# Kernel optimization log

Measured on AMD Instinct MI355X. Metric: run time of the kernel, lower is better.

The kernel has to match this reference:

```python
import jax, jax.numpy as jnp
import numpy as np

# static config (matches init_kwargs)
B = 16
S = 32          # patch grid side
td = 2          # tile_dim
ts = td * td    # tile size
T = (S // td) ** 2
R = 1           # register tokens
U = 1           # tile_comp_size
P = S * S
N = R + P
KC = T * U
K = R + KC
D = 768
H = 12
DH = D // H
HID = 32        # CPB hidden


def setup_inputs() -> dict:
    key = jax.random.key(0)
    ks = jax.random.split(key, 11)
    sc = 0.02
    x = jax.random.normal(ks[0], (B, N, D), jnp.float32)
    logit_w = jax.random.normal(ks[1], (U, D), jnp.float32) * sc
    q_w = jax.random.normal(ks[2], (D, D), jnp.float32) * sc
    kv_w = jax.random.normal(ks[3], (2 * D, D), jnp.float32) * sc
    out_w = jax.random.normal(ks[4], (D, D), jnp.float32) * sc
    out_b = jax.random.normal(ks[5], (D,), jnp.float32) * sc
    cpb_w1 = jax.random.normal(ks[6], (HID, 3), jnp.float32) * 0.5
    cpb_b1 = jax.random.normal(ks[7], (HID,), jnp.float32) * sc
    cpb_w2 = jax.random.normal(ks[8], (H, HID), jnp.float32) * 0.1
    cpb_b2 = jax.random.normal(ks[9], (H,), jnp.float32) * sc
    u_pos = jax.random.normal(ks[10], (1, U, 3), jnp.float32) * sc
    # query patch positions [qx, qy, 0] on the SxS grid (row-major)
    coords = np.arange(S, dtype=np.float32)
    gy, gx = np.meshgrid(coords, coords, indexing='ij')
    P_pos = np.stack([gx.ravel(), gy.ravel(), np.zeros(P, np.float32)], axis=-1)[:, None, :]
    # per-tile centers [cx, cy, 0], tile index t = row_tile*(S//td)+col_tile
    tc = np.arange(S // td, dtype=np.float32) * td + (td - 1) / 2.0
    ty, tx = np.meshgrid(tc, tc, indexing='ij')
    tile_centers = np.stack([tx.ravel(), ty.ravel(), np.zeros(T, np.float32)], axis=-1)[:, None, :]
    return {
        'x': x, 'logit_w': logit_w, 'q_w': q_w, 'kv_w': kv_w,
        'out_w': out_w, 'out_b': out_b,
        'cpb_w1': cpb_w1, 'cpb_b1': cpb_b1, 'cpb_w2': cpb_w2, 'cpb_b2': cpb_b2,
        'u_pos': u_pos,
        'P_pos': jnp.asarray(P_pos), 'tile_centers': jnp.asarray(tile_centers),
    }


def _cpb_bias(P_pos, tile_centers, u_pos, cpb_w1, cpb_b1, cpb_w2, cpb_b2, dtype):
    # anchors: tile center + tied per-U offset -> [KC, 3]
    k_pos = (tile_centers + u_pos).reshape(KC, 3)
    delta = P_pos - k_pos[None, :, :].reshape(1, KC, 3)  # [P, KC, 3]
    dxy, s_feat = delta[..., :2], delta[..., 2:]
    phi_xy = jnp.sign(dxy) * jnp.log1p(jnp.abs(dxy))
    feats = jnp.concatenate([phi_xy, -s_feat], axis=-1)  # [P, KC, 3]
    h = jax.nn.gelu(feats @ cpb_w1.T + cpb_b1, approximate=False)
    out_ctx = h @ cpb_w2.T + cpb_b2  # [P, KC, H]
    bias = jnp.zeros((N, K, H), dtype).at[R:, R:, :].set(out_ctx.astype(dtype))
    return bias.transpose(2, 0, 1)  # [H, N, K]


def reference(x, logit_w, q_w, kv_w, out_w, out_b,
              cpb_w1, cpb_b1, cpb_w2, cpb_b2, u_pos, P_pos, tile_centers):
    Bx = x.shape[0]
    # --- tiled softmax-weighted compression ---
    patch = x[:, R:, :].reshape(Bx, S // td, td, S // td, td, D)
    tiled = patch.transpose(0, 1, 3, 2, 4, 5).reshape(Bx, T, ts, D)  # [B,T,ts,D]
    scores = jnp.einsum('btsd,ud->btsu', tiled, logit_w)             # [B,T,ts,U]
    w = jax.nn.softmax(scores.astype(jnp.float32).transpose(0, 1, 3, 2), axis=-1)
    w = w.astype(scores.dtype)                                       # [B,T,U,ts]
    ctx_learn = jnp.einsum('btus,btsd->btud', w, tiled).reshape(Bx, T * U, D)
    ctx = jnp.concatenate([x[:, :R, :], ctx_learn], axis=1)          # [B,K,D]
    # --- projections ---
    q = jnp.einsum('bnd,ed->bne', x, q_w).reshape(Bx, N, H, DH).transpose(0, 2, 1, 3)
    kv = jnp.einsum('bkd,ed->bke', ctx, kv_w).reshape(Bx, K, 2, H, DH)
    k = kv[:, :, 0].transpose(0, 2, 1, 3)  # [B,H,K,DH]
    v = kv[:, :, 1].transpose(0, 2, 1, 3)
    # --- CPB additive bias + SDPA ---
    bias = _cpb_bias(P_pos, tile_centers, u_pos, cpb_w1, cpb_b1, cpb_w2, cpb_b2, x.dtype)
    scale = DH ** -0.5
    logits = jnp.einsum('bhnd,bhkd->bhnk', q, k) * scale + bias[None]
    attn = jax.nn.softmax(logits, axis=-1)
    o = jnp.einsum('bhnk,bhkd->bhnd', attn, v).transpose(0, 2, 1, 3).reshape(Bx, N, D)
    return o @ out_w.T + out_b
```

## Files before the change

### kernel.cpp

```cpp
#include <hip/hip_runtime.h>
#include <math.h>

namespace {
constexpr int BB   = 16;
constexpr int SS   = 32;
constexpr int TT   = 256;
constexpr int PP   = 1024;
constexpr int NTOK = 1025;
constexpr int KCC  = 256;
constexpr int KTOK = 257;
constexpr int DD   = 768;
constexpr int HH   = 12;
constexpr int DHH  = 64;
constexpr int BNP  = 1040;
}

typedef _Float16 f16x8 __attribute__((ext_vector_type(8)));
typedef _Float16 f16x2 __attribute__((ext_vector_type(2)));
typedef float f32x4 __attribute__((ext_vector_type(4)));

#define GLOAD_LDS16(gsrc, ldst)                                               \
  __builtin_amdgcn_global_load_lds(                                           \
      (const __attribute__((address_space(1))) unsigned int*)(gsrc),          \
      (__attribute__((address_space(3))) unsigned int*)(ldst), 16, 0, 0)

__global__ __launch_bounds__(256) void cvt_weights_kernel(
    const float* __restrict__ q_w, const float* __restrict__ kv_w,
    const float* __restrict__ out_w,
    _Float16* __restrict__ qwh, _Float16* __restrict__ kvwh,
    _Float16* __restrict__ owh) {
  constexpr int NQ = DD * DD;
  constexpr int NK = 2 * DD * DD;
  const int i = (blockIdx.x * 256 + threadIdx.x) * 8;
  const float* src;
  _Float16* dst;
  int off;
  float scale = 1.0f;
  if (i < NQ) { src = q_w; dst = qwh; off = i; scale = 0.125f; }
  else if (i < NQ + NK) { src = kv_w; dst = kvwh; off = i - NQ; }
  else if (i < NQ + NK + NQ) { src = out_w; dst = owh; off = i - NQ - NK; }
  else return;
  const float4 a = *(const float4*)(src + off);
  const float4 b = *(const float4*)(src + off + 4);
  f16x8 o;
  o[0] = (_Float16)(a.x * scale); o[1] = (_Float16)(a.y * scale);
  o[2] = (_Float16)(a.z * scale); o[3] = (_Float16)(a.w * scale);
  o[4] = (_Float16)(b.x * scale); o[5] = (_Float16)(b.y * scale);
  o[6] = (_Float16)(b.z * scale); o[7] = (_Float16)(b.w * scale);
  *(f16x8*)(dst + off) = o;
}

__global__ __launch_bounds__(256) void ctx_kernel(
    const float* __restrict__ x, const float* __restrict__ logit_w,
    _Float16* __restrict__ ctxh, _Float16* __restrict__ xh) {
  const int blk = blockIdx.x;
  const int b = blk >> 8;
  const int t = blk & 255;
  const int tid = threadIdx.x;
  const int lane = tid & 63;
  const int w = tid >> 6;
  const float* xb = x + (size_t)b * NTOK * DD;
  _Float16* xhb = xh + (size_t)b * NTOK * DD;

  int prow[4];
#pragma unroll
  for (int s = 0; s < 4; ++s)
    prow[s] = 1 + ((t >> 4) * 2 + (s >> 1)) * SS + ((t & 15) * 2 + (s & 1));

  float sv[3][4];
  float part[4] = {0.f, 0.f, 0.f, 0.f};
#pragma unroll
  for (int it = 0; it < 3; ++it) {
    const int d = tid + 256 * it;
    const float lw = logit_w[d];
#pragma unroll
    for (int s = 0; s < 4; ++s) {
      const float xv = xb[(size_t)prow[s] * DD + d];
      sv[it][s] = xv;
      part[s] += xv * lw;
      xhb[(size_t)prow[s] * DD + d] = (_Float16)xv;
    }
  }

#pragma unroll
  for (int dd = 1; dd < 64; dd <<= 1)
#pragma unroll
    for (int s = 0; s < 4; ++s) part[s] += __shfl_xor(part[s], dd, 64);
  __shared__ float wred[4][4];
  if (lane == 0)
#pragma unroll
    for (int s = 0; s < 4; ++s) wred[w][s] = part[s];
  __syncthreads();
  float score[4];
#pragma unroll
  for (int s = 0; s < 4; ++s)
    score[s] = wred[0][s] + wred[1][s] + wred[2][s] + wred[3][s];

  const float mx = fmaxf(fmaxf(score[0], score[1]), fmaxf(score[2], score[3]));
  float e[4], sum = 0.f;
#pragma unroll
  for (int s = 0; s < 4; ++s) { e[s] = expf(score[s] - mx); sum += e[s]; }
  const float inv = 1.f / sum;
#pragma unroll
  for (int s = 0; s < 4; ++s) e[s] *= inv;

  _Float16* crow = ctxh + ((size_t)b * KTOK + 1 + t) * DD;
#pragma unroll
  for (int it = 0; it < 3; ++it) {
    const int d = tid + 256 * it;
    float acc = 0.f;
#pragma unroll
    for (int s = 0; s < 4; ++s) acc += e[s] * sv[it][s];
    crow[d] = (_Float16)acc;
  }
  if (t == 0) {
    _Float16* dst = ctxh + (size_t)b * KTOK * DD;
#pragma unroll
    for (int it = 0; it < 3; ++it) {
      const int d = tid + 256 * it;
      const float xv = xb[d];
      dst[d] = (_Float16)xv;
      xhb[d] = (_Float16)xv;
    }
  }
}

template <int OUTF16>
__global__ __launch_bounds__(256) void gemm_f16_kernel(
    const _Float16* __restrict__ A, const _Float16* __restrict__ W,
    const float* __restrict__ bias, void* __restrict__ Cout,
    int M, int Nout, int gx) {
  constexpr int BK = 64;
  __shared__ _Float16 As[128 * BK];
  __shared__ _Float16 Ws[128 * BK];

  const int tid = threadIdx.x;
  const int lane = tid & 63;
  const int w = tid >> 6;
  const int fr = lane & 15;
  const int g = lane >> 4;
  const int awm = (w >> 1) * 64;
  const int awn = (w & 1) * 64;

  const int nwg = gridDim.x;
  const int q8 = nwg >> 3, r8 = nwg & 7;
  const int xcd = blockIdx.x & 7;
  const int base = (xcd < r8) ? xcd * (q8 + 1) : r8 * (q8 + 1) + (xcd - r8) * q8;
  const int wg = base + (blockIdx.x >> 3);
  const int row0 = (wg / gx) * 128;
  const int col0 = (wg % gx) * 128;

  const int srow = lane >> 3;
  const int schunk = (lane & 7) ^ (srow & 7);

  f32x4 acc[4][4];
#pragma unroll
  for (int i = 0; i < 4; ++i)
#pragma unroll
    for (int j = 0; j < 4; ++j) acc[i][j] = (f32x4){0.f, 0.f, 0.f, 0.f};

  for (int k0 = 0; k0 < 768; k0 += BK) {
    __syncthreads();
#pragma unroll
    for (int c = 0; c < 4; ++c) {
      const int rl = w * 32 + c * 8 + srow;
      int ga = row0 + rl;
      ga = ga < M ? ga : M - 1;
      GLOAD_LDS16(A + (size_t)ga * 768 + k0 + schunk * 8, &As[(w * 32 + c * 8) * BK]);
      GLOAD_LDS16(W + (size_t)(col0 + rl) * 768 + k0 + schunk * 8,
                  &Ws[(w * 32 + c * 8) * BK]);
    }
    __syncthreads();

#pragma unroll
    for (int ks = 0; ks < 2; ++ks) {
      f16x8 af[4], bf[4];
#pragma unroll
      for (int i = 0; i < 4; ++i) {
        const int row = awm + i * 16 + fr;
        af[i] = *(const f16x8*)&As[row * BK + (((ks * 4 + g) ^ (fr & 7)) * 8)];
      }
#pragma unroll
      for (int j = 0; j < 4; ++j) {
        const int row = awn + j * 16 + fr;
        bf[j] = *(const f16x8*)&Ws[row * BK + (((ks * 4 + g) ^ (fr & 7)) * 8)];
      }
#pragma unroll
      for (int i = 0; i < 4; ++i)
#pragma unroll
        for (int j = 0; j < 4; ++j)
          acc[i][j] = __builtin_amdgcn_mfma_f32_16x16x32_f16(af[i], bf[j], acc[i][j], 0, 0, 0);
    }
  }

#pragma unroll
  for (int i = 0; i < 4; ++i) {
    const int rbase = row0 + awm + i * 16 + g * 4;
#pragma unroll
    for (int reg = 0; reg < 4; ++reg) {
      const int gr = rbase + reg;
      if (gr >= M) continue;
      if constexpr (OUTF16) {
        _Float16* crow = (_Float16*)Cout + (size_t)gr * Nout + col0;
#pragma unroll
        for (int j = 0; j < 4; ++j)
          crow[awn + j * 16 + fr] = (_Float16)acc[i][j][reg];
      } else {
        float* crow = (float*)Cout + (size_t)gr * Nout + col0;
#pragma unroll
        for (int j = 0; j < 4; ++j) {
          const int gc = awn + j * 16 + fr;
          crow[gc] = acc[i][j][reg] + bias[col0 + gc];
        }
      }
    }
  }
}

__global__ __launch_bounds__(256) void cpb_kernel(
    const float* __restrict__ P_pos, const float* __restrict__ tile_centers,
    const float* __restrict__ u_pos,
    const float* __restrict__ w1, const float* __restrict__ b1,
    const float* __restrict__ w2, const float* __restrict__ b2,
    float* __restrict__ biasK) {
  const int idx = blockIdx.x * 256 + threadIdx.x;
  const int c = idx >> 10;
  const int p = idx & 1023;

  const float px = P_pos[p * 3 + 0], py = P_pos[p * 3 + 1], pz = P_pos[p * 3 + 2];
  const float kx = tile_centers[c * 3 + 0] + u_pos[0];
  const float ky = tile_centers[c * 3 + 1] + u_pos[1];
  const float kz = tile_centers[c * 3 + 2] + u_pos[2];
  const float dx = px - kx, dy = py - ky, dz = pz - kz;
  const float fx = copysignf(log1pf(fabsf(dx)), dx);
  const float fy = copysignf(log1pf(fabsf(dy)), dy);
  const float fz = -dz;

  float outh[HH];
#pragma unroll
  for (int h = 0; h < HH; ++h) outh[h] = b2[h];
  for (int j = 0; j < 32; ++j) {
    float hj = fx * w1[j * 3 + 0] + fy * w1[j * 3 + 1] + fz * w1[j * 3 + 2] + b1[j];
    hj = 0.5f * hj * (1.f + erff(hj * 0.70710678118654752f));
#pragma unroll
    for (int h = 0; h < HH; ++h) outh[h] += hj * w2[h * 32 + j];
  }
#pragma unroll
  for (int h = 0; h < HH; ++h) {
    float* row = biasK + ((size_t)h * KCC + c) * BNP;
    row[1 + p] = outh[h];
    if (p == 0) row[0] = 0.f;
    if (p < BNP - 1 - PP) row[1 + PP + p] = 0.f;
  }
}

__global__ __launch_bounds__(512) void attn_mfma_kernel(
    const _Float16* __restrict__ qf, const _Float16* __restrict__ kvf,
    const float* __restrict__ biasK, _Float16* __restrict__ of) {
  __shared__ _Float16 Kh[4][64 * 64];
  __shared__ _Float16 Vt[4][64 * 64];
  __shared__ _Float16 Pl[8][16 * 64];

  const int tid = threadIdx.x;
  const int lane = tid & 63;
  const int w = tid >> 6;
  const int fr = lane & 15;
  const int g = lane >> 4;

  const int xcd = blockIdx.x & 7;
  const int s = blockIdx.x >> 3;
  const int grp = xcd + 8 * (s >> 1);
  const int half = s & 1;
  const int b = grp / HH;
  const int h = grp % HH;

  if (tid < 256) {
    const int ksr = tid >> 2;
    const int kc0 = (tid & 3) * 2;
    const int s7 = ksr & 7;
#pragma unroll
    for (int kt = 0; kt < 4; ++kt) {
      const int key = kt * 64 + ksr;
      const _Float16* srcK = kvf + ((size_t)b * KTOK + key) * (2 * DD) + h * DHH;
      *(f16x8*)&Kh[kt][ksr * 64 + ((kc0 ^ s7) * 8)] = *(const f16x8*)(srcK + kc0 * 8);
      *(f16x8*)&Kh[kt][ksr * 64 + (((kc0 + 1) ^ s7) * 8)] = *(const f16x8*)(srcK + kc0 * 8 + 8);
    }
  } else {
    const int t2 = tid - 256;
    const int vkp = t2 & 31;
    const int vdh = (t2 >> 5) * 8;
#pragma unroll
    for (int kt = 0; kt < 4; ++kt) {
      const int kv0 = kt * 64 + 2 * vkp;
      const f16x8 va = *(const f16x8*)(kvf + ((size_t)b * KTOK + kv0) * (2 * DD) + DD + h * DHH + vdh);
      const f16x8 vbv = *(const f16x8*)(kvf + ((size_t)b * KTOK + kv0 + 1) * (2 * DD) + DD + h * DHH + vdh);
#pragma unroll
      for (int e = 0; e < 8; ++e) {
        const int d = vdh + e;
        f16x2 pr; pr[0] = va[e]; pr[1] = vbv[e];
        *(f16x2*)&Vt[kt][d * 64 + (((vkp >> 2) ^ (d & 7)) * 8) + 2 * (vkp & 3)] = pr;
      }
    }
  }

  const _Float16* k256p = kvf + ((size_t)b * KTOK + 256) * (2 * DD) + h * DHH;
  f16x8 kt256[2];
#pragma unroll
  for (int ks = 0; ks < 2; ++ks)
    kt256[ks] = *(const f16x8*)(k256p + ks * 32 + g * 8);
  float v256[4];
#pragma unroll
  for (int j = 0; j < 4; ++j) v256[j] = (float)k256p[DD + j * 16 + fr];

  __syncthreads();

  const int cstart = half ? 33 : 0;
  const int cend = half ? 65 : 33;
  for (int c = cstart + w; c < cend; c += 8) {
    const int qc = c * 16;

    const int qrow = min(qc + fr, NTOK - 1);
    const _Float16* qsrc = qf + ((size_t)b * NTOK + qrow) * DD + h * DHH;
    f16x8 qa[2];
#pragma unroll
    for (int ks = 0; ks < 2; ++ks)
      qa[ks] = *(const f16x8*)(qsrc + ks * 32 + g * 8);

    float mr_[4], lr_[4];
#pragma unroll
    for (int r = 0; r < 4; ++r) { mr_[r] = -3.0e38f; lr_[r] = 0.f; }
    f32x4 outacc[4];
#pragma unroll
    for (int j = 0; j < 4; ++j) outacc[j] = (f32x4){0.f, 0.f, 0.f, 0.f};

    const int nb = min(qc + g * 4, PP);

#pragma unroll
    for (int kt = 0; kt < 4; ++kt) {
      const int k0 = kt * 64;
      f32x4 sf[4];
      __builtin_amdgcn_s_setprio(1);
#pragma unroll
      for (int f = 0; f < 4; ++f) {
        sf[f] = (f32x4){0.f, 0.f, 0.f, 0.f};
#pragma unroll
        for (int ks = 0; ks < 2; ++ks) {
          const f16x8 kf = *(const f16x8*)&Kh[kt][(f * 16 + fr) * 64 + (((ks * 4 + g) ^ (fr & 7)) * 8)];
          sf[f] = __builtin_amdgcn_mfma_f32_16x16x32_f16(qa[ks], kf, sf[f], 0, 0, 0);
        }
      }
      __builtin_amdgcn_s_setprio(0);

      float pm[4][4];
#pragma unroll
      for (int f = 0; f < 4; ++f) {
        const int key = k0 + f * 16 + fr;
        const int cl = min(max(key - 1, 0), KCC - 1);
        const f32x4 b4 = *(const f32x4*)&biasK[((size_t)h * KCC + cl) * BNP + nb];
        const float bm = (key >= 1) ? 1.f : 0.f;
#pragma unroll
        for (int r = 0; r < 4; ++r) pm[f][r] = sf[f][r] + bm * b4[r];
      }

#pragma unroll
      for (int r = 0; r < 4; ++r) {
        float rm = fmaxf(fmaxf(pm[0][r], pm[1][r]), fmaxf(pm[2][r], pm[3][r]));
#pragma unroll
        for (int d = 1; d < 16; d <<= 1) rm = fmaxf(rm, __shfl_xor(rm, d, 64));
        const float mn = fmaxf(mr_[r], rm);
        const float corr = __expf(mr_[r] - mn);
        mr_[r] = mn;
        float rs = 0.f;
#pragma unroll
        for (int f = 0; f < 4; ++f) {
          const float pv = __expf(pm[f][r] - mn);
          pm[f][r] = pv;
          rs += pv;
        }
#pragma unroll
        for (int d = 1; d < 16; d <<= 1) rs += __shfl_xor(rs, d, 64);
        lr_[r] = lr_[r] * corr + rs;
#pragma unroll
        for (int j = 0; j < 4; ++j) outacc[j][r] *= corr;
      }

#pragma unroll
      for (int f = 0; f < 4; ++f)
#pragma unroll
        for (int r = 0; r < 4; ++r) {
          const int prw = g * 4 + r;
          Pl[w][prw * 64 + (((2 * f + (fr >> 3)) ^ (prw & 7)) * 8) + (fr & 7)] =
              (_Float16)pm[f][r];
        }

      __builtin_amdgcn_s_setprio(1);
#pragma unroll
      for (int ks = 0; ks < 2; ++ks) {
        const f16x8 pa = *(const f16x8*)&Pl[w][fr * 64 + (((ks * 4 + g) ^ (fr & 7)) * 8)];
#pragma unroll
        for (int j = 0; j < 4; ++j) {
          const f16x8 vbf = *(const f16x8*)&Vt[kt][(j * 16 + fr) * 64 + (((ks * 4 + g) ^ (fr & 7)) * 8)];
          outacc[j] = __builtin_amdgcn_mfma_f32_16x16x32_f16(pa, vbf, outacc[j], 0, 0, 0);
        }
      }
      __builtin_amdgcn_s_setprio(0);
    }

    {
      float sp = 0.f;
#pragma unroll
      for (int ks = 0; ks < 2; ++ks)
#pragma unroll
        for (int j = 0; j < 8; ++j)
          sp += (float)qa[ks][j] * (float)kt256[ks][j];
      sp += __shfl_xor(sp, 16, 64);
      sp += __shfl_xor(sp, 32, 64);
      const f32x4 bt = *(const f32x4*)&biasK[((size_t)h * KCC + (KCC - 1)) * BNP + nb];
#pragma unroll
      for (int r = 0; r < 4; ++r) {
        const float s256 = __shfl(sp, g * 4 + r, 64) + bt[r];
        const float mn = fmaxf(mr_[r], s256);
        const float corr = __expf(mr_[r] - mn);
        const float pv = __expf(s256 - mn);
        mr_[r] = mn;
        lr_[r] = lr_[r] * corr + pv;
#pragma unroll
        for (int j = 0; j < 4; ++j)
          outacc[j][r] = outacc[j][r] * corr + pv * v256[j];
      }
    }

#pragma unroll
    for (int r = 0; r < 4; ++r) {
      const int n = qc + g * 4 + r;
      if (n >= NTOK) continue;
      const float inv = 1.f / lr_[r];
      _Float16* orow = of + ((size_t)b * NTOK + n) * DD + h * DHH + fr;
#pragma unroll
      for (int j = 0; j < 4; ++j) orow[j * 16] = (_Float16)(outacc[j][r] * inv);
    }
  }
}

extern "C" void kernel_launch(void* const* d_in, const int* in_sizes, int n_in,
                              void* d_out, int out_size, void* d_ws, size_t ws_size,
                              hipStream_t stream) {
  const float* x            = (const float*)d_in[0];
  const float* logit_w      = (const float*)d_in[1];
  const float* q_w          = (const float*)d_in[2];
  const float* kv_w         = (const float*)d_in[3];
  const float* out_w        = (const float*)d_in[4];
  const float* out_b        = (const float*)d_in[5];
  const float* cpb_w1       = (const float*)d_in[6];
  const float* cpb_b1       = (const float*)d_in[7];
  const float* cpb_w2       = (const float*)d_in[8];
  const float* cpb_b2       = (const float*)d_in[9];
  const float* u_pos        = (const float*)d_in[10];
  const float* P_pos        = (const float*)d_in[11];
  const float* tile_centers = (const float*)d_in[12];
  float* out = (float*)d_out;

  const int Mq  = BB * NTOK;
  const int Mkv = BB * KTOK;

  char* p = (char*)d_ws;
  auto alloc = [&](size_t bytes) {
    char* r = p;
    p += (bytes + 255) & ~(size_t)255;
    return r;
  };
  _Float16* xh    = (_Float16*)alloc((size_t)Mq * DD * 2);
  _Float16* ctxh  = (_Float16*)alloc((size_t)Mkv * DD * 2);
  _Float16* qwh   = (_Float16*)alloc((size_t)DD * DD * 2);
  _Float16* kvwh  = (_Float16*)alloc((size_t)2 * DD * DD * 2);
  _Float16* owh   = (_Float16*)alloc((size_t)DD * DD * 2);
  _Float16* qbuf  = (_Float16*)alloc((size_t)Mq * DD * 2);
  _Float16* kvbuf = (_Float16*)alloc((size_t)Mkv * 2 * DD * 2);
  float*    biasK = (float*)alloc((size_t)HH * KCC * BNP * 4);
  _Float16* obuf  = (_Float16*)alloc((size_t)Mq * DD * 2);

  const int n_wt = 4 * DD * DD;

  cvt_weights_kernel<<<(n_wt / 8 + 255) / 256, 256, 0, stream>>>(
      q_w, kv_w, out_w, qwh, kvwh, owh);

  ctx_kernel<<<BB * TT, 256, 0, stream>>>(x, logit_w, ctxh, xh);

  const int gq = 6 * 129;
  const int gk = 12 * 33;
  gemm_f16_kernel<1><<<gq, 256, 0, stream>>>(xh, qwh, nullptr, qbuf, Mq, DD, 6);
  gemm_f16_kernel<1><<<gk, 256, 0, stream>>>(ctxh, kvwh, nullptr, kvbuf, Mkv, 2 * DD, 12);

  cpb_kernel<<<(PP * KCC) / 256, 256, 0, stream>>>(
      P_pos, tile_centers, u_pos, cpb_w1, cpb_b1, cpb_w2, cpb_b2, biasK);

  attn_mfma_kernel<<<2 * BB * HH, 512, 0, stream>>>(qbuf, kvbuf, biasK, obuf);

  gemm_f16_kernel<0><<<gq, 256, 0, stream>>>(obuf, owh, out_b, out, Mq, DD, 6);
}
```

Before: 206.1 us.

## Replace online softmax with single-pass full-row softmax and halve attention grid

The attention kernel now computes all 256 key scores for a query chunk at once and takes the row max and sum in one pass, instead of keeping a running max with correction factors per key tile. The 257th key's contribution is folded in at the final write. The grid drops from two blocks per batch-head (split over query chunks) to one block that loops over all 65 chunks. This removes the per-tile rescale, exp and shuffle work, at the cost of more registers held for the score array and half as many blocks to fill the GPU.

Result: faster. 175.4 us (median of 3 runs) (-14.9%).

```diff
diff --git a/kernel.cpp b/kernel.cpp
--- a/kernel.cpp
+++ b/kernel.cpp
@@ -268,9 +268,7 @@
   const int g = lane >> 4;
 
   const int xcd = blockIdx.x & 7;
-  const int s = blockIdx.x >> 3;
-  const int grp = xcd + 8 * (s >> 1);
-  const int half = s & 1;
+  const int grp = xcd + 8 * (blockIdx.x >> 3);
   const int b = grp / HH;
   const int h = grp % HH;
 
@@ -314,9 +312,7 @@
 
   __syncthreads();
 
-  const int cstart = half ? 33 : 0;
-  const int cend = half ? 65 : 33;
-  for (int c = cstart + w; c < cend; c += 8) {
+  for (int c = w; c < 65; c += 8) {
     const int qc = c * 16;
 
     const int qrow = min(qc + fr, NTOK - 1);
@@ -326,73 +322,85 @@
     for (int ks = 0; ks < 2; ++ks)
       qa[ks] = *(const f16x8*)(qsrc + ks * 32 + g * 8);
 
-    float mr_[4], lr_[4];
-#pragma unroll
-    for (int r = 0; r < 4; ++r) { mr_[r] = -3.0e38f; lr_[r] = 0.f; }
-    f32x4 outacc[4];
-#pragma unroll
-    for (int j = 0; j < 4; ++j) outacc[j] = (f32x4){0.f, 0.f, 0.f, 0.f};
-
     const int nb = min(qc + g * 4, PP);
 
+    float sp = 0.f;
+#pragma unroll
+    for (int ks = 0; ks < 2; ++ks)
+#pragma unroll
+      for (int j = 0; j < 8; ++j)
+        sp += (float)qa[ks][j] * (float)kt256[ks][j];
+    sp += __shfl_xor(sp, 16, 64);
+    sp += __shfl_xor(sp, 32, 64);
+    const f32x4 bt = *(const f32x4*)&biasK[((size_t)h * KCC + (KCC - 1)) * BNP + nb];
+
+    float sm[4][4][4];
+    __builtin_amdgcn_s_setprio(1);
 #pragma unroll
     for (int kt = 0; kt < 4; ++kt) {
-      const int k0 = kt * 64;
-      f32x4 sf[4];
-      __builtin_amdgcn_s_setprio(1);
 #pragma unroll
       for (int f = 0; f < 4; ++f) {
-        sf[f] = (f32x4){0.f, 0.f, 0.f, 0.f};
+        f32x4 sf = (f32x4){0.f, 0.f, 0.f, 0.f};
 #pragma unroll
         for (int ks = 0; ks < 2; ++ks) {
           const f16x8 kf = *(const f16x8*)&Kh[kt][(f * 16 + fr) * 64 + (((ks * 4 + g) ^ (fr & 7)) * 8)];
-          sf[f] = __builtin_amdgcn_mfma_f32_16x16x32_f16(qa[ks], kf, sf[f], 0, 0, 0);
+          sf = __builtin_amdgcn_mfma_f32_16x16x32_f16(qa[ks], kf, sf, 0, 0, 0);
         }
-      }
-      __builtin_amdgcn_s_setprio(0);
-
-      float pm[4][4];
-#pragma unroll
-      for (int f = 0; f < 4; ++f) {
-        const int key = k0 + f * 16 + fr;
+        const int key = kt * 64 + f * 16 + fr;
         const int cl = min(max(key - 1, 0), KCC - 1);
         const f32x4 b4 = *(const f32x4*)&biasK[((size_t)h * KCC + cl) * BNP + nb];
         const float bm = (key >= 1) ? 1.f : 0.f;
 #pragma unroll
-        for (int r = 0; r < 4; ++r) pm[f][r] = sf[f][r] + bm * b4[r];
-      }
-
-#pragma unroll
-      for (int r = 0; r < 4; ++r) {
-        float rm = fmaxf(fmaxf(pm[0][r], pm[1][r]), fmaxf(pm[2][r], pm[3][r]));
-#pragma unroll
-        for (int d = 1; d < 16; d <<= 1) rm = fmaxf(rm, __shfl_xor(rm, d, 64));
-        const float mn = fmaxf(mr_[r], rm);
-        const float corr = __expf(mr_[r] - mn);
-        mr_[r] = mn;
-        float rs = 0.f;
+        for (int r = 0; r < 4; ++r) sm[kt][f][r] = sf[r] + bm * b4[r];
+      }
+    }
+    __builtin_amdgcn_s_setprio(0);
+
+    float lr_[4], p256[4];
+#pragma unroll
+    for (int r = 0; r < 4; ++r) {
+      float m01 = fmaxf(sm[0][0][r], sm[0][1][r]);
+      float m23 = fmaxf(sm[0][2][r], sm[0][3][r]);
+#pragma unroll
+      for (int kt = 1; kt < 4; ++kt) {
+        m01 = fmaxf(m01, fmaxf(sm[kt][0][r], sm[kt][1][r]));
+        m23 = fmaxf(m23, fmaxf(sm[kt][2][r], sm[kt][3][r]));
+      }
+      float m = fmaxf(m01, m23);
+#pragma unroll
+      for (int d = 1; d < 16; d <<= 1) m = fmaxf(m, __shfl_xor(m, d, 64));
+      const float s256r = __shfl(sp, g * 4 + r, 64) + bt[r];
+      m = fmaxf(m, s256r);
+
+      float rs = 0.f;
+#pragma unroll
+      for (int kt = 0; kt < 4; ++kt)
 #pragma unroll
         for (int f = 0; f < 4; ++f) {
-          const float pv = __expf(pm[f][r] - mn);
-          pm[f][r] = pv;
+          const float pv = __expf(sm[kt][f][r] - m);
+          sm[kt][f][r] = pv;
           rs += pv;
         }
 #pragma unroll
-        for (int d = 1; d < 16; d <<= 1) rs += __shfl_xor(rs, d, 64);
-        lr_[r] = lr_[r] * corr + rs;
-#pragma unroll
-        for (int j = 0; j < 4; ++j) outacc[j][r] *= corr;
-      }
-
+      for (int d = 1; d < 16; d <<= 1) rs += __shfl_xor(rs, d, 64);
+      p256[r] = __expf(s256r - m);
+      lr_[r] = rs + p256[r];
+    }
+
+    f32x4 outacc[4];
+#pragma unroll
+    for (int j = 0; j < 4; ++j) outacc[j] = (f32x4){0.f, 0.f, 0.f, 0.f};
+
+#pragma unroll
+    for (int kt = 0; kt < 4; ++kt) {
 #pragma unroll
       for (int f = 0; f < 4; ++f)
 #pragma unroll
         for (int r = 0; r < 4; ++r) {
           const int prw = g * 4 + r;
           Pl[w][prw * 64 + (((2 * f + (fr >> 3)) ^ (prw & 7)) * 8) + (fr & 7)] =
-              (_Float16)pm[f][r];
+              (_Float16)sm[kt][f][r];
         }
-
       __builtin_amdgcn_s_setprio(1);
 #pragma unroll
       for (int ks = 0; ks < 2; ++ks) {
@@ -404,30 +412,6 @@
         }
       }
       __builtin_amdgcn_s_setprio(0);
-    }
-
-    {
-      float sp = 0.f;
-#pragma unroll
-      for (int ks = 0; ks < 2; ++ks)
-#pragma unroll
-        for (int j = 0; j < 8; ++j)
-          sp += (float)qa[ks][j] * (float)kt256[ks][j];
-      sp += __shfl_xor(sp, 16, 64);
-      sp += __shfl_xor(sp, 32, 64);
-      const f32x4 bt = *(const f32x4*)&biasK[((size_t)h * KCC + (KCC - 1)) * BNP + nb];
-#pragma unroll
-      for (int r = 0; r < 4; ++r) {
-        const float s256 = __shfl(sp, g * 4 + r, 64) + bt[r];
-        const float mn = fmaxf(mr_[r], s256);
-        const float corr = __expf(mr_[r] - mn);
-        const float pv = __expf(s256 - mn);
-        mr_[r] = mn;
-        lr_[r] = lr_[r] * corr + pv;
-#pragma unroll
-        for (int j = 0; j < 4; ++j)
-          outacc[j][r] = outacc[j][r] * corr + pv * v256[j];
-      }
     }
 
 #pragma unroll
@@ -437,7 +421,8 @@
       const float inv = 1.f / lr_[r];
       _Float16* orow = of + ((size_t)b * NTOK + n) * DD + h * DHH + fr;
 #pragma unroll
-      for (int j = 0; j < 4; ++j) orow[j * 16] = (_Float16)(outacc[j][r] * inv);
+      for (int j = 0; j < 4; ++j)
+        orow[j * 16] = (_Float16)((outacc[j][r] + p256[r] * v256[j]) * inv);
     }
   }
 }
@@ -494,7 +479,7 @@
   cpb_kernel<<<(PP * KCC) / 256, 256, 0, stream>>>(
       P_pos, tile_centers, u_pos, cpb_w1, cpb_b1, cpb_w2, cpb_b2, biasK);
 
-  attn_mfma_kernel<<<2 * BB * HH, 512, 0, stream>>>(qbuf, kvbuf, biasK, obuf);
+  attn_mfma_kernel<<<BB * HH, 512, 0, stream>>>(qbuf, kvbuf, biasK, obuf);
 
   gemm_f16_kernel<0><<<gq, 256, 0, stream>>>(obuf, owh, out_b, out, Mq, DD, 6);
 }
```
